# Kernel tuning notes

Measured on AMD Instinct MI355X. Metric: run time of the kernel, lower is better.

Reference implementation:

```python
import jax, jax.numpy as jnp
import numpy as np

B, S, E, H = 4, 1024, 768, 12
DH = E // H  # per-head dim = 64
PRIOR_VAR = 0.01


def _kl(mu, logvar):
    # kl_regularizer from the source: logvar (units,) broadcasts against mu (in,units)
    t = (jnp.log(PRIOR_VAR) - 1.0 - logvar
         + jnp.log1p(jnp.exp(logvar)) / PRIOR_VAR
         + mu * mu / PRIOR_VAR)
    return 0.5 * jnp.mean(t)


def _linear_first(x, w_mu, w_sigma):
    mu = x @ w_mu
    W_Sigma = jnp.log1p(jnp.exp(w_sigma))            # softplus(w_sigma)
    xs = x / x.shape[-1]                              # x / dim (dim = last dim of x)
    xx = jnp.sum(xs * xs, axis=-1, keepdims=True)     # [B,S,1]
    Sigma = jax.nn.softplus(xx * W_Sigma)             # [B,S,E]
    return mu, Sigma, _kl(w_mu, w_sigma)


def _linear_not_first(mu_in, Sigma_in, w_mu, w_sigma):
    mu = mu_in @ w_mu
    W_Sigma = jnp.log1p(jnp.exp(w_sigma))
    wm = w_mu / jnp.sqrt(jnp.float32(w_mu.shape[0]))  # w_mu / sqrt(in_dim)
    S1 = Sigma_in @ (wm * wm)                         # w^T Sigma_in w
    xs = mu_in / mu_in.shape[-1]
    S2 = jnp.sum(xs * xs, axis=-1, keepdims=True) * W_Sigma
    S3 = jnp.sum(Sigma_in, axis=-1, keepdims=True) * W_Sigma / W_Sigma.shape[-1]
    Sigma = jax.nn.softplus(S1 + S2 + S3)
    return mu, Sigma, _kl(w_mu, w_sigma)


def _heads(x):
    # [B,S,E] -> [B,H,S,DH]
    return x.reshape(B, S, H, DH).transpose(0, 2, 1, 3)


def setup_inputs() -> dict:
    key = jax.random.key(0)
    ks = jax.random.split(key, 9)
    glorot = lambda k: jax.random.normal(k, (E, E), jnp.float32) * jnp.sqrt(2.0 / (E + E))
    sig = lambda k: jax.random.uniform(k, (E,), jnp.float32, minval=-4.6, maxval=-2.25)
    return {
        "x": jax.random.normal(ks[0], (B, S, E), jnp.float32),
        "wq_mu": glorot(ks[1]), "wq_sigma": sig(ks[2]),
        "wk_mu": glorot(ks[3]), "wk_sigma": sig(ks[4]),
        "wv_mu": glorot(ks[5]), "wv_sigma": sig(ks[6]),
        "wo_mu": glorot(ks[7]), "wo_sigma": sig(ks[8]),
    }


def reference(x, wq_mu, wq_sigma, wk_mu, wk_sigma, wv_mu, wv_sigma, wo_mu, wo_sigma):
    # dropout is identity in eval mode (training=False)
    mq, sq, klq = _linear_first(x, wq_mu, wq_sigma)
    mk, sk, klk = _linear_first(x, wk_mu, wk_sigma)
    mv, sv, klv = _linear_first(x, wv_mu, wv_sigma)
    mq, sq, mk, sk, mv, sv = map(_heads, (mq, sq, mk, sk, mv, sv))

    dk = jnp.float32(DH)
    mu_score = jnp.einsum('bhqd,bhkd->bhqk', mq, mk)
    a = jnp.einsum('bhqd,bhkd->bhqk', mq * mq / dk, sk)
    b = jnp.einsum('bhqd,bhkd->bhqk', mk * mk / dk, sq)   # matmul(mk^2/dk, sq^T) as in TF source
    c = jnp.einsum('bhqd,bhkd->bhqk', sq / jnp.sqrt(dk), sk / jnp.sqrt(dk))
    sigma_score = a + b + c

    mu_scaled = mu_score / jnp.sqrt(dk)
    sigma_scaled = sigma_score / dk
    w = jax.nn.softmax(mu_scaled, axis=-1)               # [B,H,S,S]
    wd = jnp.float32(S)
    grad = (w - w * w) ** 2
    Sw = grad * sigma_scaled / wd

    mu_att = jnp.einsum('bhqk,bhkd->bhqd', w, mv)
    d = jnp.einsum('bhqk,bhkd->bhqd', w * w / wd, sv)
    e = jnp.einsum('bhqk,bhkd->bhqd', Sw, mv * mv / wd)
    f = jnp.einsum('bhqk,bhkd->bhqd', Sw / jnp.sqrt(wd), sv / jnp.sqrt(wd))
    sig_att = jax.nn.softplus(d + e + f)

    mu_cat = mu_att.transpose(0, 2, 1, 3).reshape(B, S, E)
    sig_cat = sig_att.transpose(0, 2, 1, 3).reshape(B, S, E)

    mu_out, Sigma_out, klo = _linear_not_first(mu_cat, sig_cat, wo_mu, wo_sigma)
    Sigma_out = jax.nn.softplus(Sigma_out)               # extra softplus in call()
    kl = klq + klk + klv + klo
    return mu_out, Sigma_out, kl
```

## Files before the change

kernel.cpp:

```cpp
#include <hip/hip_runtime.h>
#include <math.h>

#define EN 768
#define SN 1024
#define HN 12
#define BSN 4096
#define BSE 3145728

#define AS1 __attribute__((address_space(1)))
#define AS3 __attribute__((address_space(3)))

typedef __attribute__((ext_vector_type(8))) short bf16x8;
typedef __attribute__((ext_vector_type(4))) float f32x4;
typedef __attribute__((ext_vector_type(4))) unsigned short u16x4;
typedef __attribute__((ext_vector_type(4))) unsigned int u32x4;
typedef unsigned short u16;

#define OFF_XX   0u
#define OFF_RC   16384u
#define OFF_WSIG 32768u
#define OFF_KL   45056u
#define OFF_ZI   49152u
#define OFF_WT   262144u
#define OFF_QH   4980736u
#define OFF_KH   11272192u
#define OFF_SQD  17563648u
#define OFF_SKD  23855104u
#define OFF_MVT  30146560u
#define OFF_MV2  36438016u
#define OFF_SVT  42729472u
#define OFF_MUH  49020928u
#define OFF_SGH  55312384u
#define OFF_WT2  61603840u

__device__ __forceinline__ float sp_f(float x){
  return fmaxf(x, 0.f) + log1pf(__expf(-fabsf(x)));
}
__device__ __forceinline__ u16 f2b(float f){
  unsigned u = __float_as_uint(f);
  return (u16)((u + 0x7fffu + ((u>>16)&1u)) >> 16);
}
__device__ __forceinline__ float b2f(u16 h){
  return __uint_as_float(((unsigned)h)<<16);
}
__device__ __forceinline__ unsigned cvtpk(float lo, float hi){
  unsigned r;
  asm("v_cvt_pk_bf16_f32 %0, %1, %2" : "=v"(r) : "v"(lo), "v"(hi));
  return r;
}
__device__ __forceinline__ bf16x8 u2b(u32x4 v){
  union{u32x4 u; bf16x8 b;} x; x.u = v; return x.b;
}
__device__ __forceinline__ f32x4 mfma16(bf16x8 a, bf16x8 b, f32x4 c){
  return __builtin_amdgcn_mfma_f32_16x16x32_bf16(a, b, c, 0, 0, 0);
}
__device__ __forceinline__ bf16x8 ldsr(const u16* t, int row, int sg){
  int a16 = (row<<3) + (sg ^ (row&7));
  return *(const bf16x8*)(t + (a16<<3));
}
__device__ __forceinline__ void stage64(u16* dst, const u16* src, int rstride, int tid){
  #pragma unroll
  for (int it=0; it<2; ++it){
    int idx = (it<<8) + tid;
    int row = idx>>3, seg = idx&7;
    bf16x8 v = *(const bf16x8*)(src + (long)row*rstride + (seg<<3));
    int a16 = (row<<3) + (seg ^ (row&7));
    *(bf16x8*)(dst + (a16<<3)) = v;
  }
}
__device__ __forceinline__ void gstage(u16* ltile, const u16* gsrc, long rstride,
                                       int w, int l){
  #pragma unroll
  for (int i=0;i<2;++i){
    int slot = (i<<8) + (w<<6) + l;
    int row  = slot >> 3;
    int seg  = (slot & 7) ^ (row & 7);
    const u16* g = gsrc + (long)row*rstride + (seg<<3);
    u16* d = ltile + (((i<<8) + (w<<6))<<3);
    __builtin_amdgcn_global_load_lds((AS1 void*)g, (AS3 void*)d, 16, 0, 0);
  }
}

__device__ __forceinline__ float blk_reduce(float v, float* tmp){
  #pragma unroll
  for (int off = 32; off; off >>= 1) v += __shfl_down(v, off, 64);
  int w = threadIdx.x >> 6;
  if ((threadIdx.x & 63) == 0) tmp[w] = v;
  __syncthreads();
  float r = 0.f;
  if (threadIdx.x == 0) r = tmp[0] + tmp[1] + tmp[2] + tmp[3];
  __syncthreads();
  return r;
}

__global__ void k_prep(const float* __restrict__ s0, const float* __restrict__ s1,
                       const float* __restrict__ s2, const float* __restrict__ s3,
                       float* __restrict__ wsig, float* __restrict__ klacc){
  __shared__ float tmp[4];
  const float* src = (blockIdx.x==0)?s0:(blockIdx.x==1)?s1:(blockIdx.x==2)?s2:s3;
  int l = blockIdx.x;
  float ssum=0.f, spsum=0.f;
  for (int j=threadIdx.x; j<EN; j+=256){
    float sg = src[j];
    float w  = log1pf(__expf(sg));
    wsig[l*EN+j] = w;
    ssum += sg; spsum += w;
  }
  float a = blk_reduce(ssum, tmp);
  float b = blk_reduce(spsum, tmp);
  if (threadIdx.x==0){ atomicAdd(&klacc[1], a); atomicAdd(&klacc[2], b); }
}

__global__ void k_xx(const float* __restrict__ x, float* __restrict__ xx){
  __shared__ float tmp[4];
  int r = blockIdx.x;
  const float* xr = x + (long)r*EN;
  float s=0.f;
  for (int j=threadIdx.x; j<EN; j+=256){ float v = xr[j]; s += v*v; }
  float t = blk_reduce(s, tmp);
  if (threadIdx.x==0) xx[r] = t*(1.0f/589824.0f);
}

__global__ void k_mu2(const float* __restrict__ w0, const float* __restrict__ w1,
                      const float* __restrict__ w2, const float* __restrict__ w3,
                      float* __restrict__ klacc){
  __shared__ float tmp[4];
  const float* w = (blockIdx.y==0)?w0:(blockIdx.y==1)?w1:(blockIdx.y==2)?w2:w3;
  const float4* w4 = (const float4*)w;
  float s=0.f;
  for (int i=blockIdx.x*256+threadIdx.x; i<147456; i+=gridDim.x*256){
    float4 v = w4[i];
    s += v.x*v.x + v.y*v.y + v.z*v.z + v.w*v.w;
  }
  float r = blk_reduce(s, tmp);
  if (threadIdx.x==0) atomicAdd(&klacc[0], r);
}

__global__ void k_wt(const float* __restrict__ w0, const float* __restrict__ w1,
                     const float* __restrict__ w2, const float* __restrict__ w3,
                     u16* __restrict__ wt, u16* __restrict__ wt2){
  __shared__ float t[64*65];
  const float* W = (blockIdx.z==0)?w0:(blockIdx.z==1)?w1:(blockIdx.z==2)?w2:w3;
  u16* WT = wt + (long)blockIdx.z*589824;
  int r0 = blockIdx.y<<6, c0 = blockIdx.x<<6;
  int tid = threadIdx.x;
  #pragma unroll
  for (int it=0; it<16; ++it){
    int idx=(it<<8)+tid; int r=idx>>6, c=idx&63;
    t[c*65+r] = W[(long)(r0+r)*EN + c0+c];
  }
  __syncthreads();
  #pragma unroll
  for (int it=0; it<16; ++it){
    int idx=(it<<8)+tid; int c=idx>>6, r=idx&63;
    u16 bb = f2b(t[c*65+r]);
    WT[(long)(c0+c)*EN + r0+r] = bb;
    if (blockIdx.z == 3){
      float bf = b2f(bb);
      wt2[(long)(c0+c)*EN + r0+r] = f2b(bf*bf);
    }
  }
}

__global__ void k_sigarr(const float* __restrict__ xx, const float* __restrict__ wsig,
                         u16* __restrict__ sqd, u16* __restrict__ skd){
  int r = blockIdx.x;
  float xr = xx[r];
  for (int c=threadIdx.x; c<EN; c+=256){
    sqd[(long)r*EN+c] = f2b(sp_f(xr*wsig[c])*(1.0f/64.0f));
    skd[(long)r*EN+c] = f2b(sp_f(xr*wsig[EN+c])*(1.0f/64.0f));
  }
}

__global__ void k_svt(const float* __restrict__ xx, const float* __restrict__ wsig,
                      u16* __restrict__ svT){
  __shared__ float sxx[64], swv[64];
  int kt=blockIdx.x, h=blockIdx.y, b=blockIdx.z, tid=threadIdx.x;
  if (tid < 64){
    sxx[tid] = xx[(long)b*SN + (kt<<6) + tid];
    swv[tid] = wsig[2*EN + (h<<6) + tid];
  }
  __syncthreads();
  long obase = (((long)(b*HN+h))<<6)*SN + (kt<<6);
  #pragma unroll
  for (int it=0; it<16; ++it){
    int idx=(it<<8)+tid; int d=idx>>6, k=idx&63;
    svT[obase + (long)d*SN + k] = f2b(sp_f(sxx[k]*swv[d]));
  }
}

__global__ __launch_bounds__(256)
void k_projmm(const float* __restrict__ x, const u16* __restrict__ WT,
              u16* __restrict__ oq, u16* __restrict__ ok,
              u16* __restrict__ mvT, u16* __restrict__ mv2T){
  __shared__ __align__(16) u16 lds[8192];
  u16* At = lds; u16* Bt = lds + 4096;
  const int tid = threadIdx.x;
  const int w = tid>>6, l = tid&63, l15 = l&15, g = l>>4;
  const int m0 = blockIdx.y<<6, n0 = blockIdx.x<<6;
  const u16* Wt = WT + (long)blockIdx.z*589824;
  f32x4 acc[4];
  #pragma unroll
  for (int t=0;t<4;++t){ acc[t][0]=0;acc[t][1]=0;acc[t][2]=0;acc[t][3]=0; }
  for (int k0=0; k0<EN; k0+=64){
    __syncthreads();
    #pragma unroll
    for (int it=0; it<2; ++it){
      int idx=(it<<8)+tid; int row=idx>>3, seg=idx&7;
      const float* sp = x + (long)(m0+row)*EN + k0 + (seg<<3);
      float4 a = *(const float4*)sp; float4 c = *(const float4*)(sp+4);
      bf16x8 v;
      v[0]=(short)f2b(a.x); v[1]=(short)f2b(a.y); v[2]=(short)f2b(a.z); v[3]=(short)f2b(a.w);
      v[4]=(short)f2b(c.x); v[5]=(short)f2b(c.y); v[6]=(short)f2b(c.z); v[7]=(short)f2b(c.w);
      int a16=(row<<3)+(seg^(row&7));
      *(bf16x8*)(At + (a16<<3)) = v;
    }
    stage64(Bt, Wt + (long)n0*EN + k0, EN, tid);
    __syncthreads();
    #pragma unroll
    for (int s=0;s<2;++s){
      int sg=(s<<2)+g;
      bf16x8 af = ldsr(At, (w<<4)+l15, sg);
      #pragma unroll
      for (int t=0;t<4;++t)
        acc[t] = mfma16(af, ldsr(Bt,(t<<4)+l15,sg), acc[t]);
    }
  }
  if (blockIdx.z < 2){
    u16* out = blockIdx.z ? ok : oq;
    #pragma unroll
    for (int t=0;t<4;++t){
      int col = n0 + (t<<4) + l15;
      #pragma unroll
      for (int r=0;r<4;++r){
        long row = m0 + (w<<4) + (g<<2) + r;
        out[row*EN + col] = f2b(acc[t][r]);
      }
    }
  } else {
    int b  = m0 >> 10;
    int hh = n0 >> 6;
    long obase = (((long)(b*HN+hh))<<6)*SN;
    int tok0 = (m0 & 1023) + (w<<4) + (g<<2);
    #pragma unroll
    for (int t=0;t<4;++t){
      int d = (t<<4) + l15;
      u16x4 m4, s4;
      #pragma unroll
      for (int r=0;r<4;++r){
        u16 mb = f2b(acc[t][r]);
        m4[r] = mb;
        float mf = b2f(mb);
        s4[r] = f2b(mf*mf);
      }
      *(u16x4*)&mvT[obase + (long)d*SN + tok0]  = m4;
      *(u16x4*)&mv2T[obase + (long)d*SN + tok0] = s4;
    }
  }
}

__global__ __launch_bounds__(512)
void k_z(const u16* __restrict__ qh, const u16* __restrict__ kh,
         float* __restrict__ zi){
  __shared__ __align__(16) u16 Tk[4096];
  const int tid = threadIdx.x;
  const int w = tid>>6, l = tid&63, l15 = l&15, g = l>>4;
  const int i = blockIdx.x;
  const int xcd = i & 7, slot = i >> 3;
  const int qt = slot & 7;
  const int pair = xcd*6 + (slot >> 3);
  const int h = pair % HN, b = pair / HN;
  const int q0 = qt<<7;
  const long bS = (long)b*SN;
  bf16x8 amq[2];
  {
    long qrow = (bS + q0 + (w<<4) + l15) * EN;
    #pragma unroll
    for (int s=0;s<2;++s)
      amq[s] = *(const bf16x8*)(qh + qrow + (h<<6) + (s<<5) + (g<<3));
  }
  const u16* khb = kh + bS*EN + (h<<6);
  const int srow = tid>>3, sseg = tid&7;
  const int a16o = (((srow<<3) + (sseg ^ (srow&7)))<<3);
  bf16x8 pf = *(const bf16x8*)(khb + (long)srow*EN + (sseg<<3));
  f32x4 zacc = {0.f,0.f,0.f,0.f};
  for (int kt=0; kt<16; ++kt){
    __syncthreads();
    *(bf16x8*)(Tk + a16o) = pf;
    __syncthreads();
    if (kt < 15)
      pf = *(const bf16x8*)(khb + (long)(((kt+1)<<6)+srow)*EN + (sseg<<3));
    f32x4 smu[4];
    #pragma unroll
    for (int t=0;t<4;++t){ smu[t][0]=0;smu[t][1]=0;smu[t][2]=0;smu[t][3]=0; }
    #pragma unroll
    for (int s=0;s<2;++s){
      int sg=(s<<2)+g;
      #pragma unroll
      for (int t=0;t<4;++t)
        smu[t] = mfma16(amq[s], ldsr(Tk,(t<<4)+l15,sg), smu[t]);
    }
    #pragma unroll
    for (int t=0;t<4;++t)
      #pragma unroll
      for (int r=0;r<4;++r)
        zacc[r] += __expf(smu[t][r]*0.125f);
  }
  #pragma unroll
  for (int m=1; m<16; m<<=1){
    #pragma unroll
    for (int r=0;r<4;++r) zacc[r] += __shfl_xor(zacc[r], m, 64);
  }
  if (l15 == 0){
    long zbase = (((long)(b*HN+h))<<10) + q0 + (w<<4) + (g<<2);
    #pragma unroll
    for (int r=0;r<4;++r) zi[zbase + r] = 1.0f/zacc[r];
  }
}

__global__ __launch_bounds__(256, 2)
void k_attn(const u16* __restrict__ qh, const u16* __restrict__ kh,
            const u16* __restrict__ sqd, const u16* __restrict__ skd,
            const u16* __restrict__ mvT, const u16* __restrict__ svT,
            const u16* __restrict__ mv2T, const float* __restrict__ zi,
            u16* __restrict__ muh, u16* __restrict__ sgh){
  extern __shared__ u16 lds2[];
  u16* Tk  = lds2;
  u16* Tsk = lds2 + 4096;
  u16* Tsq = lds2 + 8192;
  u16* Tmv = lds2 + 12288;
  u16* Tsv = lds2 + 16384;
  u16* Tm2 = lds2 + 20480;
  const int tid = threadIdx.x;
  const int w = tid>>6, l = tid&63, l15 = l&15, g = l>>4;
  unsigned* Pu = (unsigned*)(lds2 + 24576) + (w<<11);
  const int ib = blockIdx.x;
  const int xcd = ib & 7, slot = ib >> 3;
  const int qt = slot & 7;
  const int pair = xcd*6 + (slot >> 3);
  const int h = pair % HN, b = pair / HN;
  const int q0 = qt<<7;
  const long bS = (long)b*SN;

  bf16x8 amq[2][2], acb[2][2], amk2[2][2];
  #pragma unroll
  for (int p=0;p<2;++p){
    long qrow = (bS + q0 + (w<<5) + (p<<4) + l15) * EN;
    #pragma unroll
    for (int s=0;s<2;++s){
      int eoff = (h<<6) + (s<<5) + (g<<3);
      bf16x8 q8 = *(const bf16x8*)(qh + qrow + eoff);
      bf16x8 k8 = *(const bf16x8*)(kh + qrow + eoff);
      bf16x8 s8 = *(const bf16x8*)(sqd + qrow + eoff);
      amq[p][s] = q8;
      bf16x8 t2, tc;
      #pragma unroll
      for (int j=0;j<8;++j){
        float kv = b2f((u16)k8[j]);
        t2[j] = (short)f2b(kv*kv);
        float qv = b2f((u16)q8[j]);
        float sv = b2f((u16)s8[j]) * 64.0f;
        tc[j] = (short)f2b(qv*qv + sv);
      }
      amk2[p][s] = t2; acb[p][s] = tc;
    }
  }
  f32x4 zl[2];
  #pragma unroll
  for (int p=0;p<2;++p){
    long zbase = (((long)(b*HN+h))<<10) + q0 + (w<<5) + (p<<4) + (g<<2);
    #pragma unroll
    for (int r=0;r<4;++r) zl[p][r] = zi[zbase + r];
  }

  const u16* khb = kh  + bS*EN + (h<<6);
  const u16* skb = skd + bS*EN + (h<<6);
  const u16* sqb = sqd + bS*EN + (h<<6);
  const long hb64 = ((long)(b*HN+h))<<6;
  const u16* mvb = mvT  + hb64*SN;
  const u16* svb = svT  + hb64*SN;
  const u16* m2b = mv2T + hb64*SN;

  f32x4 accM[2][4], acc2[2][4], acc3[2][4];
  #pragma unroll
  for (int p=0;p<2;++p)
    #pragma unroll
    for (int t=0;t<4;++t){
      accM[p][t][0]=0;accM[p][t][1]=0;accM[p][t][2]=0;accM[p][t][3]=0;
      acc2[p][t][0]=0;acc2[p][t][1]=0;acc2[p][t][2]=0;acc2[p][t][3]=0;
      acc3[p][t][0]=0;acc3[p][t][1]=0;acc3[p][t][2]=0;acc3[p][t][3]=0;
    }

  gstage(Tk,  khb, EN, w, l);
  gstage(Tsk, skb, EN, w, l);
  gstage(Tsq, sqb, EN, w, l);

  for (int kt=0; kt<16; ++kt){
    __syncthreads();
    gstage(Tmv, mvb + (kt<<6), SN, w, l);
    gstage(Tsv, svb + (kt<<6), SN, w, l);
    gstage(Tm2, m2b + (kt<<6), SN, w, l);

    #pragma unroll
    for (int t=0;t<4;++t){
      f32x4 smu[2], ssg[2];
      #pragma unroll
      for (int p=0;p<2;++p){
        smu[p][0]=0;smu[p][1]=0;smu[p][2]=0;smu[p][3]=0;
        ssg[p][0]=0;ssg[p][1]=0;ssg[p][2]=0;ssg[p][3]=0;
      }
      int rn = (t<<4)+l15;
      #pragma unroll
      for (int s=0;s<2;++s){
        int sg=(s<<2)+g;
        bf16x8 bk = ldsr(Tk, rn, sg);
        bf16x8 bs = ldsr(Tsk,rn, sg);
        bf16x8 bq = ldsr(Tsq,rn, sg);
        #pragma unroll
        for (int p=0;p<2;++p){
          smu[p] = mfma16(amq[p][s],  bk, smu[p]);
          ssg[p] = mfma16(acb[p][s],  bs, ssg[p]);
          ssg[p] = mfma16(amk2[p][s], bq, ssg[p]);
        }
      }
      #pragma unroll
      for (int p=0;p<2;++p){
        #pragma unroll
        for (int r=0;r<4;++r){
          float e  = __expf(smu[p][r]*0.125f);
          float wv = e*zl[p][r];
          float u  = wv - wv*wv;
          float sw = u*u*ssg[p][r]*(1.0f/65536.0f);
          int prow = (g<<2)+r, pcol = (t<<4)+l15;
          int a32 = (p<<10) + ((((prow<<3) + ((pcol>>3)^(prow&7)))<<3) + (pcol&7));
          Pu[a32] = cvtpk(wv, sw);
        }
      }
    }
    __syncthreads();
    if (kt < 15){
      long o1 = (long)((kt+1)<<6)*EN;
      gstage(Tk,  khb + o1, EN, w, l);
      gstage(Tsk, skb + o1, EN, w, l);
      gstage(Tsq, sqb + o1, EN, w, l);
    }
    #pragma unroll
    for (int s=0;s<2;++s){
      int sg=(s<<2)+g;
      bf16x8 aw[2], ag[2], pa[2];
      #pragma unroll
      for (int p=0;p<2;++p){
        const u32x4* pp = (const u32x4*)(Pu + (p<<10) + (((l15<<3) + (sg ^ (l15&7)))<<3));
        u32x4 pA = pp[0], pB = pp[1];
        unsigned qa[8] = {pA[0],pA[1],pA[2],pA[3],pB[0],pB[1],pB[2],pB[3]};
        u32x4 awu, agu, pau;
        #pragma unroll
        for (int i2=0;i2<4;++i2){
          unsigned lo = qa[2*i2], hi = qa[2*i2+1];
          awu[i2] = (lo & 0xffffu) | (hi << 16);
          agu[i2] = (lo >> 16) | (hi & 0xffff0000u);
          float w0 = __uint_as_float(lo<<16), g0 = __uint_as_float(lo & 0xffff0000u);
          float w1 = __uint_as_float(hi<<16), g1 = __uint_as_float(hi & 0xffff0000u);
          pau[i2] = cvtpk(fmaf(w0,w0,g0), fmaf(w1,w1,g1));
        }
        aw[p]=u2b(awu); ag[p]=u2b(agu); pa[p]=u2b(pau);
      }
      #pragma unroll
      for (int t=0;t<4;++t){
        int rn = (t<<4)+l15;
        bf16x8 bm  = ldsr(Tmv,rn,sg);
        bf16x8 bv  = ldsr(Tsv,rn,sg);
        bf16x8 b2m = ldsr(Tm2,rn,sg);
        #pragma unroll
        for (int p=0;p<2;++p){
          accM[p][t] = mfma16(aw[p], bm,  accM[p][t]);
          acc2[p][t] = mfma16(pa[p], bv,  acc2[p][t]);
          acc3[p][t] = mfma16(ag[p], b2m, acc3[p][t]);
        }
      }
    }
  }
  #pragma unroll
  for (int p=0;p<2;++p){
    long grow0 = bS + q0 + (w<<5) + (p<<4) + (g<<2);
    #pragma unroll
    for (int t=0;t<4;++t){
      int col = (h<<6) + (t<<4) + l15;
      #pragma unroll
      for (int r=0;r<4;++r){
        long o = (grow0 + r)*EN + col;
        muh[o] = f2b(accM[p][t][r]);
        sgh[o] = f2b(sp_f((acc2[p][t][r]+acc3[p][t][r])*(1.0f/1024.0f)));
      }
    }
  }
}

__global__ void k_rows(const u16* __restrict__ muh, const u16* __restrict__ sgh,
                       float* __restrict__ rcomb){
  __shared__ float tmp[4];
  int r = blockIdx.x;
  const u16* m = muh + (long)r*EN;
  const u16* s = sgh + (long)r*EN;
  float s1=0.f, s2=0.f;
  for (int j=threadIdx.x; j<EN; j+=256){ float a=b2f(m[j]); s1+=a*a; s2+=b2f(s[j]); }
  float r1 = blk_reduce(s1, tmp);
  float r2 = blk_reduce(s2, tmp);
  if (threadIdx.x==0) rcomb[r] = r1*(1.0f/589824.0f) + r2*(1.0f/768.0f);
}

__global__ __launch_bounds__(256)
void k_outmm(const u16* __restrict__ muh, const u16* __restrict__ sgh,
             const u16* __restrict__ WTo, const u16* __restrict__ WT2o,
             const float* __restrict__ rcomb, const float* __restrict__ wso,
             float* __restrict__ mu_out, float* __restrict__ sg_out){
  __shared__ __align__(16) u16 lds[16384];
  u16* Am = lds; u16* As = lds + 4096; u16* Bt = lds + 8192; u16* B2t = lds + 12288;
  const int tid = threadIdx.x;
  const int w = tid>>6, l = tid&63, l15 = l&15, g = l>>4;
  const int m0 = blockIdx.y<<6, n0 = blockIdx.x<<6;
  f32x4 accM[4], accS[4];
  #pragma unroll
  for (int t=0;t<4;++t){
    accM[t][0]=0;accM[t][1]=0;accM[t][2]=0;accM[t][3]=0;
    accS[t][0]=0;accS[t][1]=0;accS[t][2]=0;accS[t][3]=0;
  }
  for (int k0=0; k0<EN; k0+=64){
    __syncthreads();
    stage64(Am, muh + (long)m0*EN + k0, EN, tid);
    stage64(As, sgh + (long)m0*EN + k0, EN, tid);
    stage64(Bt, WTo + (long)n0*EN + k0, EN, tid);
    stage64(B2t, WT2o + (long)n0*EN + k0, EN, tid);
    __syncthreads();
    #pragma unroll
    for (int s=0;s<2;++s){
      int sg=(s<<2)+g;
      bf16x8 am = ldsr(Am, (w<<4)+l15, sg);
      bf16x8 as = ldsr(As, (w<<4)+l15, sg);
      #pragma unroll
      for (int t=0;t<4;++t){
        int rn=(t<<4)+l15;
        accM[t] = mfma16(am, ldsr(Bt,rn,sg), accM[t]);
        accS[t] = mfma16(as, ldsr(B2t,rn,sg), accS[t]);
      }
    }
  }
  float rc4[4];
  #pragma unroll
  for (int r=0;r<4;++r) rc4[r] = rcomb[m0 + (w<<4) + (g<<2) + r];
  #pragma unroll
  for (int t=0;t<4;++t){
    int col = n0 + (t<<4) + l15;
    float wsc = wso[col];
    #pragma unroll
    for (int r=0;r<4;++r){
      long row = m0 + (w<<4) + (g<<2) + r;
      mu_out[row*EN + col] = accM[t][r];
      float spre = accS[t][r]*(1.0f/768.0f) + rc4[r]*wsc;
      sg_out[row*EN + col] = sp_f(sp_f(spre));
    }
  }
}

__global__ void k_klf(const float* __restrict__ klacc, float* __restrict__ out){
  float Smu2 = klacc[0], Ssig = klacc[1], Ssp = klacc[2];
  const float C = -5.60517018599f;
  out[0] = 0.5f*(4.f*C - Ssig*(1.0f/768.0f) + Ssp*(1.0f/7.68f) + Smu2*(1.0f/5898.24f));
}

extern "C" void kernel_launch(void* const* d_in, const int* in_sizes, int n_in,
                              void* d_out, int out_size, void* d_ws, size_t ws_size,
                              hipStream_t stream) {
  (void)in_sizes; (void)n_in; (void)out_size; (void)ws_size;
  const float* x      = (const float*)d_in[0];
  const float* wq_mu  = (const float*)d_in[1];
  const float* wq_sig = (const float*)d_in[2];
  const float* wk_mu  = (const float*)d_in[3];
  const float* wk_sig = (const float*)d_in[4];
  const float* wv_mu  = (const float*)d_in[5];
  const float* wv_sig = (const float*)d_in[6];
  const float* wo_mu  = (const float*)d_in[7];
  const float* wo_sig = (const float*)d_in[8];

  char* wsb = (char*)d_ws;
  float* xx    = (float*)(wsb + OFF_XX);
  float* rc    = (float*)(wsb + OFF_RC);
  float* wsig  = (float*)(wsb + OFF_WSIG);
  float* kla   = (float*)(wsb + OFF_KL);
  float* zi    = (float*)(wsb + OFF_ZI);
  u16*   WT    = (u16*)(wsb + OFF_WT);
  u16*   qh    = (u16*)(wsb + OFF_QH);
  u16*   kh    = (u16*)(wsb + OFF_KH);
  u16*   sqd   = (u16*)(wsb + OFF_SQD);
  u16*   skd   = (u16*)(wsb + OFF_SKD);
  u16*   mvT   = (u16*)(wsb + OFF_MVT);
  u16*   mv2T  = (u16*)(wsb + OFF_MV2);
  u16*   svT   = (u16*)(wsb + OFF_SVT);
  u16*   muh   = (u16*)(wsb + OFF_MUH);
  u16*   sgh   = (u16*)(wsb + OFF_SGH);
  u16*   WT2   = (u16*)(wsb + OFF_WT2);

  float* mu_out = (float*)d_out;
  float* sg_out = mu_out + BSE;
  float* kl_out = mu_out + 2*BSE;

  (void)hipMemsetAsync(kla, 0, 3*sizeof(float), stream);
  k_prep<<<4, 256, 0, stream>>>(wq_sig, wk_sig, wv_sig, wo_sig, wsig, kla);
  k_xx<<<BSN, 256, 0, stream>>>(x, xx);
  k_mu2<<<dim3(64,4), 256, 0, stream>>>(wq_mu, wk_mu, wv_mu, wo_mu, kla);
  k_wt<<<dim3(12,12,4), 256, 0, stream>>>(wq_mu, wk_mu, wv_mu, wo_mu, WT, WT2);
  k_sigarr<<<BSN, 256, 0, stream>>>(xx, wsig, sqd, skd);
  k_svt<<<dim3(16,HN,4), 256, 0, stream>>>(xx, wsig, svT);
  k_projmm<<<dim3(12,64,3), 256, 0, stream>>>(x, WT, qh, kh, mvT, mv2T);
  k_z<<<384, 512, 0, stream>>>(qh, kh, zi);

  const int attn_lds = 81920;
  (void)hipFuncSetAttribute((const void*)k_attn,
                      hipFuncAttributeMaxDynamicSharedMemorySize, attn_lds);
  k_attn<<<384, 256, attn_lds, stream>>>(qh, kh, sqd, skd, mvT, svT,
                                         mv2T, zi, muh, sgh);
  k_rows<<<BSN, 256, 0, stream>>>(muh, sgh, rc);
  k_outmm<<<dim3(12,64), 256, 0, stream>>>(muh, sgh, WT + 3l*589824, WT2, rc,
                                           wsig + 3*EN, mu_out, sg_out);
  k_klf<<<1, 1, 0, stream>>>(kla, kl_out);
}
```

Baseline: 341.6 us.

## Fuse prep kernels, pre-convert x to bf16, fold row sums into attention

Merges the x row-norm, the bf16 conversion of x and the sigma-array kernels into one pass, and folds the w_mu squared-sum into the transpose kernel. It also drops the k_rows kernel by reducing the row statistics inside the attention epilogue with atomics. Other changes: the projection and output GEMMs use a gstage loader, k_z reads K straight from global instead of through LDS, the P-tile LDS layout is rearranged, and sigma scaling constants are rescaled. The aim is fewer launches and less repeated global traffic, at the cost of atomics and a changed bf16 scaling that could affect precision.

```diff
diff --git a/kernel.cpp b/kernel.cpp
--- a/kernel.cpp
+++ b/kernel.cpp
@@ -33,6 +33,9 @@
 #define OFF_SGH  55312384u
 #define OFF_WT2  61603840u
 
+#define SSCL 2.384185791015625e-7f
+#define SINV 4194304.0f
+
 __device__ __forceinline__ float sp_f(float x){
   return fmaxf(x, 0.f) + log1pf(__expf(-fabsf(x)));
 }
@@ -111,45 +114,55 @@
   if (threadIdx.x==0){ atomicAdd(&klacc[1], a); atomicAdd(&klacc[2], b); }
 }
 
-__global__ void k_xx(const float* __restrict__ x, float* __restrict__ xx){
+__global__ void k_xxs(const float* __restrict__ x, const float* __restrict__ wsig,
+                      float* __restrict__ xx, u16* __restrict__ xb,
+                      u16* __restrict__ sqd, u16* __restrict__ skd){
   __shared__ float tmp[4];
-  int r = blockIdx.x;
+  __shared__ float srow[EN];
+  __shared__ float sxx;
+  int r = blockIdx.x, tid = threadIdx.x;
   const float* xr = x + (long)r*EN;
   float s=0.f;
-  for (int j=threadIdx.x; j<EN; j+=256){ float v = xr[j]; s += v*v; }
+  #pragma unroll
+  for (int it=0; it<3; ++it){
+    int j = it*256 + tid;
+    float v = xr[j];
+    srow[j] = v;
+    s += v*v;
+  }
   float t = blk_reduce(s, tmp);
-  if (threadIdx.x==0) xx[r] = t*(1.0f/589824.0f);
-}
-
-__global__ void k_mu2(const float* __restrict__ w0, const float* __restrict__ w1,
-                      const float* __restrict__ w2, const float* __restrict__ w3,
-                      float* __restrict__ klacc){
-  __shared__ float tmp[4];
-  const float* w = (blockIdx.y==0)?w0:(blockIdx.y==1)?w1:(blockIdx.y==2)?w2:w3;
-  const float4* w4 = (const float4*)w;
-  float s=0.f;
-  for (int i=blockIdx.x*256+threadIdx.x; i<147456; i+=gridDim.x*256){
-    float4 v = w4[i];
-    s += v.x*v.x + v.y*v.y + v.z*v.z + v.w*v.w;
-  }
-  float r = blk_reduce(s, tmp);
-  if (threadIdx.x==0) atomicAdd(&klacc[0], r);
+  if (tid==0){ float v = t*(1.0f/589824.0f); xx[r]=v; sxx=v; }
+  __syncthreads();
+  float xv = sxx;
+  #pragma unroll
+  for (int it=0; it<3; ++it){
+    int c = it*256 + tid;
+    xb[(long)r*EN+c]  = f2b(srow[c]);
+    sqd[(long)r*EN+c] = f2b(sp_f(xv*wsig[c])*SSCL);
+    skd[(long)r*EN+c] = f2b(sp_f(xv*wsig[EN+c])*SSCL);
+  }
 }
 
 __global__ void k_wt(const float* __restrict__ w0, const float* __restrict__ w1,
                      const float* __restrict__ w2, const float* __restrict__ w3,
-                     u16* __restrict__ wt, u16* __restrict__ wt2){
+                     u16* __restrict__ wt, u16* __restrict__ wt2,
+                     float* __restrict__ klacc){
   __shared__ float t[64*65];
+  __shared__ float tmp[4];
   const float* W = (blockIdx.z==0)?w0:(blockIdx.z==1)?w1:(blockIdx.z==2)?w2:w3;
   u16* WT = wt + (long)blockIdx.z*589824;
   int r0 = blockIdx.y<<6, c0 = blockIdx.x<<6;
   int tid = threadIdx.x;
+  float s = 0.f;
   #pragma unroll
   for (int it=0; it<16; ++it){
     int idx=(it<<8)+tid; int r=idx>>6, c=idx&63;
-    t[c*65+r] = W[(long)(r0+r)*EN + c0+c];
-  }
-  __syncthreads();
+    float v = W[(long)(r0+r)*EN + c0+c];
+    t[c*65+r] = v;
+    s += v*v;
+  }
+  float sr = blk_reduce(s, tmp);
+  if (tid==0) atomicAdd(&klacc[0], sr);
   #pragma unroll
   for (int it=0; it<16; ++it){
     int idx=(it<<8)+tid; int c=idx>>6, r=idx&63;
@@ -162,16 +175,6 @@
   }
 }
 
-__global__ void k_sigarr(const float* __restrict__ xx, const float* __restrict__ wsig,
-                         u16* __restrict__ sqd, u16* __restrict__ skd){
-  int r = blockIdx.x;
-  float xr = xx[r];
-  for (int c=threadIdx.x; c<EN; c+=256){
-    sqd[(long)r*EN+c] = f2b(sp_f(xr*wsig[c])*(1.0f/64.0f));
-    skd[(long)r*EN+c] = f2b(sp_f(xr*wsig[EN+c])*(1.0f/64.0f));
-  }
-}
-
 __global__ void k_svt(const float* __restrict__ xx, const float* __restrict__ wsig,
                       u16* __restrict__ svT){
   __shared__ float sxx[64], swv[64];
@@ -190,7 +193,7 @@
 }
 
 __global__ __launch_bounds__(256)
-void k_projmm(const float* __restrict__ x, const u16* __restrict__ WT,
+void k_projmm(const u16* __restrict__ xb, const u16* __restrict__ WT,
               u16* __restrict__ oq, u16* __restrict__ ok,
               u16* __restrict__ mvT, u16* __restrict__ mv2T){
   __shared__ __align__(16) u16 lds[8192];
@@ -204,18 +207,8 @@
   for (int t=0;t<4;++t){ acc[t][0]=0;acc[t][1]=0;acc[t][2]=0;acc[t][3]=0; }
   for (int k0=0; k0<EN; k0+=64){
     __syncthreads();
-    #pragma unroll
-    for (int it=0; it<2; ++it){
-      int idx=(it<<8)+tid; int row=idx>>3, seg=idx&7;
-      const float* sp = x + (long)(m0+row)*EN + k0 + (seg<<3);
-      float4 a = *(const float4*)sp; float4 c = *(const float4*)(sp+4);
-      bf16x8 v;
-      v[0]=(short)f2b(a.x); v[1]=(short)f2b(a.y); v[2]=(short)f2b(a.z); v[3]=(short)f2b(a.w);
-      v[4]=(short)f2b(c.x); v[5]=(short)f2b(c.y); v[6]=(short)f2b(c.z); v[7]=(short)f2b(c.w);
-      int a16=(row<<3)+(seg^(row&7));
-      *(bf16x8*)(At + (a16<<3)) = v;
-    }
-    stage64(Bt, Wt + (long)n0*EN + k0, EN, tid);
+    gstage(At, xb + (long)m0*EN + k0, EN, w, l);
+    gstage(Bt, Wt + (long)n0*EN + k0, EN, w, l);
     __syncthreads();
     #pragma unroll
     for (int s=0;s<2;++s){
@@ -259,52 +252,40 @@
   }
 }
 
-__global__ __launch_bounds__(512)
+__global__ __launch_bounds__(256)
 void k_z(const u16* __restrict__ qh, const u16* __restrict__ kh,
          float* __restrict__ zi){
-  __shared__ __align__(16) u16 Tk[4096];
   const int tid = threadIdx.x;
   const int w = tid>>6, l = tid&63, l15 = l&15, g = l>>4;
   const int i = blockIdx.x;
   const int xcd = i & 7, slot = i >> 3;
-  const int qt = slot & 7;
-  const int pair = xcd*6 + (slot >> 3);
+  const int qt = slot & 15;
+  const int pair = xcd*6 + (slot >> 4);
   const int h = pair % HN, b = pair / HN;
-  const int q0 = qt<<7;
+  const int q0 = (qt<<6) + (w<<4);
   const long bS = (long)b*SN;
   bf16x8 amq[2];
   {
-    long qrow = (bS + q0 + (w<<4) + l15) * EN;
+    long qrow = (bS + q0 + l15) * EN;
     #pragma unroll
     for (int s=0;s<2;++s)
       amq[s] = *(const bf16x8*)(qh + qrow + (h<<6) + (s<<5) + (g<<3));
   }
   const u16* khb = kh + bS*EN + (h<<6);
-  const int srow = tid>>3, sseg = tid&7;
-  const int a16o = (((srow<<3) + (sseg ^ (srow&7)))<<3);
-  bf16x8 pf = *(const bf16x8*)(khb + (long)srow*EN + (sseg<<3));
   f32x4 zacc = {0.f,0.f,0.f,0.f};
   for (int kt=0; kt<16; ++kt){
-    __syncthreads();
-    *(bf16x8*)(Tk + a16o) = pf;
-    __syncthreads();
-    if (kt < 15)
-      pf = *(const bf16x8*)(khb + (long)(((kt+1)<<6)+srow)*EN + (sseg<<3));
-    f32x4 smu[4];
-    #pragma unroll
-    for (int t=0;t<4;++t){ smu[t][0]=0;smu[t][1]=0;smu[t][2]=0;smu[t][3]=0; }
-    #pragma unroll
-    for (int s=0;s<2;++s){
-      int sg=(s<<2)+g;
-      #pragma unroll
-      for (int t=0;t<4;++t)
-        smu[t] = mfma16(amq[s], ldsr(Tk,(t<<4)+l15,sg), smu[t]);
-    }
-    #pragma unroll
-    for (int t=0;t<4;++t)
-      #pragma unroll
-      for (int r=0;r<4;++r)
-        zacc[r] += __expf(smu[t][r]*0.125f);
+    #pragma unroll
+    for (int t=0;t<4;++t){
+      f32x4 sm = {0.f,0.f,0.f,0.f};
+      #pragma unroll
+      for (int s=0;s<2;++s){
+        const bf16x8 bf = *(const bf16x8*)(khb + (long)((kt<<6)+(t<<4)+l15)*EN
+                                           + (((s<<2)+g)<<3));
+        sm = mfma16(amq[s], bf, sm);
+      }
+      #pragma unroll
+      for (int r=0;r<4;++r) zacc[r] += __expf(sm[r]*0.125f);
+    }
   }
   #pragma unroll
   for (int m=1; m<16; m<<=1){
@@ -312,7 +293,7 @@
     for (int r=0;r<4;++r) zacc[r] += __shfl_xor(zacc[r], m, 64);
   }
   if (l15 == 0){
-    long zbase = (((long)(b*HN+h))<<10) + q0 + (w<<4) + (g<<2);
+    long zbase = (((long)(b*HN+h))<<10) + q0 + (g<<2);
     #pragma unroll
     for (int r=0;r<4;++r) zi[zbase + r] = 1.0f/zacc[r];
   }
@@ -323,7 +304,8 @@
             const u16* __restrict__ sqd, const u16* __restrict__ skd,
             const u16* __restrict__ mvT, const u16* __restrict__ svT,
             const u16* __restrict__ mv2T, const float* __restrict__ zi,
-            u16* __restrict__ muh, u16* __restrict__ sgh){
+            u16* __restrict__ muh, u16* __restrict__ sgh,
+            float* __restrict__ rc){
   extern __shared__ u16 lds2[];
   u16* Tk  = lds2;
   u16* Tsk = lds2 + 4096;
@@ -359,7 +341,7 @@
         float kv = b2f((u16)k8[j]);
         t2[j] = (short)f2b(kv*kv);
         float qv = b2f((u16)q8[j]);
-        float sv = b2f((u16)s8[j]) * 64.0f;
+        float sv = b2f((u16)s8[j]) * SINV;
         tc[j] = (short)f2b(qv*qv + sv);
       }
       amk2[p][s] = t2; acb[p][s] = tc;
@@ -430,9 +412,9 @@
           float e  = __expf(smu[p][r]*0.125f);
           float wv = e*zl[p][r];
           float u  = wv - wv*wv;
-          float sw = u*u*ssg[p][r]*(1.0f/65536.0f);
-          int prow = (g<<2)+r, pcol = (t<<4)+l15;
-          int a32 = (p<<10) + ((((prow<<3) + ((pcol>>3)^(prow&7)))<<3) + (pcol&7));
+          float sw = u*u*ssg[p][r];
+          int pc3 = (t<<1) + (l15>>3);
+          int a32 = (p<<10) | (pc3<<7) | (r<<5) | (g<<3) | (l15&7);
           Pu[a32] = cvtpk(wv, sw);
         }
       }
@@ -450,7 +432,8 @@
       bf16x8 aw[2], ag[2], pa[2];
       #pragma unroll
       for (int p=0;p<2;++p){
-        const u32x4* pp = (const u32x4*)(Pu + (p<<10) + (((l15<<3) + (sg ^ (l15&7)))<<3));
+        const u32x4* pp = (const u32x4*)(Pu + ((p<<10) | (sg<<7) |
+                            ((l15&3)<<5) | ((l15>>2)<<3)));
         u32x4 pA = pp[0], pB = pp[1];
         unsigned qa[8] = {pA[0],pA[1],pA[2],pA[3],pB[0],pB[1],pB[2],pB[3]};
         u32x4 awu, agu, pau;
@@ -483,30 +466,34 @@
   #pragma unroll
   for (int p=0;p<2;++p){
     long grow0 = bS + q0 + (w<<5) + (p<<4) + (g<<2);
+    float sm2[4] = {0.f,0.f,0.f,0.f};
+    float ssm[4] = {0.f,0.f,0.f,0.f};
     #pragma unroll
     for (int t=0;t<4;++t){
       int col = (h<<6) + (t<<4) + l15;
       #pragma unroll
       for (int r=0;r<4;++r){
         long o = (grow0 + r)*EN + col;
-        muh[o] = f2b(accM[p][t][r]);
-        sgh[o] = f2b(sp_f((acc2[p][t][r]+acc3[p][t][r])*(1.0f/1024.0f)));
-      }
-    }
-  }
-}
-
-__global__ void k_rows(const u16* __restrict__ muh, const u16* __restrict__ sgh,
-                       float* __restrict__ rcomb){
-  __shared__ float tmp[4];
-  int r = blockIdx.x;
-  const u16* m = muh + (long)r*EN;
-  const u16* s = sgh + (long)r*EN;
-  float s1=0.f, s2=0.f;
-  for (int j=threadIdx.x; j<EN; j+=256){ float a=b2f(m[j]); s1+=a*a; s2+=b2f(s[j]); }
-  float r1 = blk_reduce(s1, tmp);
-  float r2 = blk_reduce(s2, tmp);
-  if (threadIdx.x==0) rcomb[r] = r1*(1.0f/589824.0f) + r2*(1.0f/768.0f);
+        float m = accM[p][t][r];
+        float sv = sp_f((acc2[p][t][r]+acc3[p][t][r])*(1.0f/1024.0f));
+        muh[o] = f2b(m);
+        sgh[o] = f2b(sv);
+        sm2[r] += m*m;
+        ssm[r] += sv;
+      }
+    }
+    #pragma unroll
+    for (int r=0;r<4;++r){
+      float a = sm2[r], c = ssm[r];
+      #pragma unroll
+      for (int off=1; off<16; off<<=1){
+        a += __shfl_xor(a, off, 16);
+        c += __shfl_xor(c, off, 16);
+      }
+      if (l15 == 0)
+        atomicAdd(&rc[grow0 + r], a*(1.0f/589824.0f) + c*(1.0f/768.0f));
+    }
+  }
 }
 
 __global__ __launch_bounds__(256)
@@ -527,10 +514,10 @@
   }
   for (int k0=0; k0<EN; k0+=64){
     __syncthreads();
-    stage64(Am, muh + (long)m0*EN + k0, EN, tid);
-    stage64(As, sgh + (long)m0*EN + k0, EN, tid);
-    stage64(Bt, WTo + (long)n0*EN + k0, EN, tid);
-    stage64(B2t, WT2o + (long)n0*EN + k0, EN, tid);
+    gstage(Am, muh + (long)m0*EN + k0, EN, w, l);
+    gstage(As, sgh + (long)m0*EN + k0, EN, w, l);
+    gstage(Bt, WTo + (long)n0*EN + k0, EN, w, l);
+    gstage(B2t, WT2o + (long)n0*EN + k0, EN, w, l);
     __syncthreads();
     #pragma unroll
     for (int s=0;s<2;++s){
@@ -599,27 +586,26 @@
   u16*   muh   = (u16*)(wsb + OFF_MUH);
   u16*   sgh   = (u16*)(wsb + OFF_SGH);
   u16*   WT2   = (u16*)(wsb + OFF_WT2);
+  u16*   xb16  = muh;
 
   float* mu_out = (float*)d_out;
   float* sg_out = mu_out + BSE;
   float* kl_out = mu_out + 2*BSE;
 
   (void)hipMemsetAsync(kla, 0, 3*sizeof(float), stream);
+  (void)hipMemsetAsync(rc, 0, BSN*sizeof(float), stream);
   k_prep<<<4, 256, 0, stream>>>(wq_sig, wk_sig, wv_sig, wo_sig, wsig, kla);
-  k_xx<<<BSN, 256, 0, stream>>>(x, xx);
-  k_mu2<<<dim3(64,4), 256, 0, stream>>>(wq_mu, wk_mu, wv_mu, wo_mu, kla);
-  k_wt<<<dim3(12,12,4), 256, 0, stream>>>(wq_mu, wk_mu, wv_mu, wo_mu, WT, WT2);
-  k_sigarr<<<BSN, 256, 0, stream>>>(xx, wsig, sqd, skd);
+  k_xxs<<<BSN, 256, 0, stream>>>(x, wsig, xx, xb16, sqd, skd);
+  k_wt<<<dim3(12,12,4), 256, 0, stream>>>(wq_mu, wk_mu, wv_mu, wo_mu, WT, WT2, kla);
   k_svt<<<dim3(16,HN,4), 256, 0, stream>>>(xx, wsig, svT);
-  k_projmm<<<dim3(12,64,3), 256, 0, stream>>>(x, WT, qh, kh, mvT, mv2T);
-  k_z<<<384, 512, 0, stream>>>(qh, kh, zi);
+  k_projmm<<<dim3(12,64,3), 256, 0, stream>>>(xb16, WT, qh, kh, mvT, mv2T);
+  k_z<<<768, 256, 0, stream>>>(qh, kh, zi);
 
   const int attn_lds = 81920;
   (void)hipFuncSetAttribute((const void*)k_attn,
                       hipFuncAttributeMaxDynamicSharedMemorySize, attn_lds);
   k_attn<<<384, 256, attn_lds, stream>>>(qh, kh, sqd, skd, mvT, svT,
-                                         mv2T, zi, muh, sgh);
-  k_rows<<<BSN, 256, 0, stream>>>(muh, sgh, rc);
+                                         mv2T, zi, muh, sgh, rc);
   k_outmm<<<dim3(12,64), 256, 0, stream>>>(muh, sgh, WT + 3l*589824, WT2, rc,
                                            wsig + 3*EN, mu_out, sg_out);
   k_klf<<<1, 1, 0, stream>>>(kla, kl_out);
```

Result: faster. 316.8 us (-7.3%).
